# Kernel tuning notes

Hardware: AMD Instinct MI355X
Metric: run time of the kernel (lower is better)

Reference implementation:

```python
import jax, jax.numpy as jnp
import numpy as np

EPS = 1e-8
ITERATIONS = 3

def squash(s):
    # s: [b, j, m]
    s2 = jnp.sum(s * s, axis=-1, keepdims=True)
    return s2 / (1.0 + s2) * (s / jnp.sqrt(s2 + EPS))

def setup_inputs() -> dict:
    key = jax.random.key(0)
    k1, k2 = jax.random.split(key)
    B, NUMS_CAPS, OUT_CAPS, IN_D, OUT_D = 128, 1152, 10, 8, 16
    x = jax.random.normal(k1, (B, NUMS_CAPS, IN_D), dtype=jnp.float32)
    w = jax.random.normal(k2, (NUMS_CAPS, OUT_CAPS, IN_D, OUT_D), dtype=jnp.float32)
    return {"nums_caps": NUMS_CAPS, "out_caps": OUT_CAPS, "x": x, "w": w}

def reference(nums_caps, out_caps, x, w):
    # x: [b, i, n], w: [i, j, n, m] -> u_hat: [b, i, j, m]
    u_hat = jnp.einsum('ijnm,bin->bijm', w, x)
    b = jnp.zeros((x.shape[0], nums_caps, out_caps), dtype=x.dtype)
    v = None
    for _ in range(ITERATIONS):
        c = jax.nn.softmax(b, axis=1)  # softmax over input capsules (dim=1, as in source)
        s = jnp.einsum('bij,bijm->bjm', c, u_hat)
        v = squash(s)
        a = jnp.einsum('bjm,bijm->bij', v, u_hat)
        b = b + a
    return v
```

## Files before the change

kernel.cpp:

```cpp
#include <hip/hip_runtime.h>
#include <hip/hip_fp16.h>


#define NB 128
#define NI 1152
#define NJ 10
#define ID 8
#define OD 16

template<int ctrl, int rmask, int bmask>
__device__ __forceinline__ float dpp_add(float x) {
    int y = __builtin_amdgcn_update_dpp(0, __builtin_bit_cast(int, x),
                                        ctrl, rmask, bmask, false);
    return x + __builtin_bit_cast(float, y);
}
__device__ __forceinline__ float wave_sum63(float x) {
    x = dpp_add<0x111, 0xf, 0xf>(x);
    x = dpp_add<0x112, 0xf, 0xf>(x);
    x = dpp_add<0x114, 0xf, 0xe>(x);
    x = dpp_add<0x118, 0xf, 0xc>(x);
    x = dpp_add<0x142, 0xa, 0xf>(x);
    x = dpp_add<0x143, 0xc, 0xf>(x);
    return x;
}

__global__ __launch_bounds__(256) void uhat_kernel(
    const float* __restrict__ x, const float* __restrict__ w,
    __half* __restrict__ uhat)
{
    __shared__ float xl[16 * 640];
    const int t  = threadIdx.x;
    const int i0 = blockIdx.x * 64;
    const int b0 = blockIdx.y * 16;
    const int j  = blockIdx.z;

    #pragma unroll
    for (int c = 0; c < 8; ++c) {
        const int h  = t + 256 * c;
        const int bb = h >> 7;
        const int ii = (h >> 1) & 63;
        const int nh = h & 1;
        const float4 xv4 = *(const float4*)(
            x + ((size_t)(b0 + bb) * NI + (i0 + ii)) * ID + nh * 4);
        float* dst = &xl[bb * 640 + ii * 10 + nh * 4];
        dst[0] = xv4.x; dst[1] = xv4.y; dst[2] = xv4.z; dst[3] = xv4.w;
    }

    const int lane = t & 63;
    const int il   = (t >> 6) * 16 + (lane >> 2);
    const int i    = i0 + il;
    const int mq   = lane & 3;

    const float* wp = w + ((size_t)i * NJ + j) * (ID * OD) + mq * 4;
    float wr[8][4];
    #pragma unroll
    for (int n = 0; n < 8; ++n)
        *(float4*)wr[n] = *(const float4*)(wp + n * OD);

    __syncthreads();

    for (int bb = 0; bb < 16; ++bb) {
        const float* xr = &xl[bb * 640 + il * 10];
        float xv[ID];
        #pragma unroll
        for (int q = 0; q < 4; ++q) { xv[2*q] = xr[2*q]; xv[2*q+1] = xr[2*q+1]; }
        float a0 = 0.f, a1 = 0.f, a2 = 0.f, a3 = 0.f;
        #pragma unroll
        for (int n = 0; n < ID; ++n) {
            a0 = fmaf(xv[n], wr[n][0], a0);
            a1 = fmaf(xv[n], wr[n][1], a1);
            a2 = fmaf(xv[n], wr[n][2], a2);
            a3 = fmaf(xv[n], wr[n][3], a3);
        }
        __half2 h01 = __floats2half2_rn(a0, a1);
        __half2 h23 = __floats2half2_rn(a2, a3);
        uint2 st;
        st.x = *(unsigned int*)&h01;
        st.y = *(unsigned int*)&h23;
        __half* up = uhat + (((size_t)(b0 + bb) * NJ + j) * NI + i) * OD + mq * 4;
        *(uint2*)up = st;
    }
}

#define P2T 192
#define P2I 6

template<int NT, int IPTT>
__device__ __forceinline__ void route_core(float (&u)[IPTT][OD], int t, int b, int j,
                                           float* __restrict__ out)
{
    constexpr int NW = NT / 64;
    __shared__ float4 red4[NW][5];
    const int wavei = t >> 6;
    const int lane  = t & 63;

    float logit[IPTT];
    #pragma unroll
    for (int k = 0; k < IPTT; ++k) logit[k] = 0.0f;
    float v[OD];

    for (int iter = 0; iter < 3; ++iter) {
        float acc[OD + 1];
        #pragma unroll
        for (int q = 0; q <= OD; ++q) acc[q] = 0.0f;
        #pragma unroll
        for (int k = 0; k < IPTT; ++k) {
            const float c = __expf(logit[k]);
            acc[OD] += c;
            #pragma unroll
            for (int m = 0; m < OD; ++m) acc[m] = fmaf(c, u[k][m], acc[m]);
        }
        #pragma unroll
        for (int q = 0; q <= OD; ++q) acc[q] = wave_sum63(acc[q]);

        if (iter != 0) __syncthreads();
        if (lane == 63) {
            red4[wavei][0] = make_float4(acc[0],  acc[1],  acc[2],  acc[3]);
            red4[wavei][1] = make_float4(acc[4],  acc[5],  acc[6],  acc[7]);
            red4[wavei][2] = make_float4(acc[8],  acc[9],  acc[10], acc[11]);
            red4[wavei][3] = make_float4(acc[12], acc[13], acc[14], acc[15]);
            red4[wavei][4] = make_float4(acc[16], 0.f, 0.f, 0.f);
        }
        __syncthreads();

        float tot[OD + 1];
        #pragma unroll
        for (int g = 0; g < 5; ++g) {
            float4 sum = red4[0][g];
            #pragma unroll
            for (int wv = 1; wv < NW; ++wv) {
                float4 r = red4[wv][g];
                sum.x += r.x; sum.y += r.y; sum.z += r.z; sum.w += r.w;
            }
            if (g < 4) {
                tot[4*g+0] = sum.x; tot[4*g+1] = sum.y;
                tot[4*g+2] = sum.z; tot[4*g+3] = sum.w;
            } else {
                tot[OD] = sum.x;
            }
        }

        const float inv_den = 1.0f / tot[OD];
        float s2 = 0.0f;
        float sv[OD];
        #pragma unroll
        for (int m = 0; m < OD; ++m) {
            sv[m] = tot[m] * inv_den;
            s2 = fmaf(sv[m], sv[m], s2);
        }
        const float scale = (s2 / (1.0f + s2)) / sqrtf(s2 + 1e-8f);
        #pragma unroll
        for (int m = 0; m < OD; ++m) v[m] = scale * sv[m];

        if (iter < 2) {
            #pragma unroll
            for (int k = 0; k < IPTT; ++k) {
                float a = 0.0f;
                #pragma unroll
                for (int m = 0; m < OD; ++m) a = fmaf(v[m], u[k][m], a);
                logit[k] += a;
            }
        }
    }
    if (t < OD) out[((size_t)b * NJ + j) * OD + t] = v[t];
}

__global__ __launch_bounds__(P2T) void route_kernel(
    const __half* __restrict__ uhat, float* __restrict__ out)
{
    const int t = threadIdx.x;
    const int b = blockIdx.x & (NB - 1);
    const int j = blockIdx.x >> 7;

    const __half* upb = uhat + ((size_t)b * NJ + j) * NI * OD;
    float u[P2I][OD];
    #pragma unroll
    for (int k = 0; k < P2I; ++k) {
        const __half* p = upb + (size_t)(t + k * P2T) * OD;
        __half2 hp[8];
        *(float4*)&hp[0] = *(const float4*)(p);
        *(float4*)&hp[4] = *(const float4*)(p + 8);
        #pragma unroll
        for (int q = 0; q < 8; ++q) {
            float2 f = __half22float2(hp[q]);
            u[k][2*q] = f.x; u[k][2*q+1] = f.y;
        }
    }
    route_core<P2T, P2I>(u, t, b, j, out);
}

__global__ __launch_bounds__(P2T) void fused_kernel(
    const float* __restrict__ x, const float* __restrict__ w,
    float* __restrict__ out)
{
    const int t = threadIdx.x;
    const int b = blockIdx.x & (NB - 1);
    const int j = blockIdx.x >> 7;

    float u[P2I][OD];
    #pragma unroll
    for (int k = 0; k < P2I; ++k) {
        const int i = t + k * P2T;
        const float* xp = x + ((size_t)b * NI + i) * ID;
        float xv[ID];
        const float4 x0 = *(const float4*)(xp);
        const float4 x1 = *(const float4*)(xp + 4);
        xv[0]=x0.x; xv[1]=x0.y; xv[2]=x0.z; xv[3]=x0.w;
        xv[4]=x1.x; xv[5]=x1.y; xv[6]=x1.z; xv[7]=x1.w;
        const float* wp = w + ((size_t)i * NJ + j) * (ID * OD);
        #pragma unroll
        for (int m = 0; m < OD; ++m) u[k][m] = 0.0f;
        #pragma unroll
        for (int n = 0; n < ID; ++n) {
            float wrow[OD];
            *(float4*)(wrow + 0)  = *(const float4*)(wp + n * OD + 0);
            *(float4*)(wrow + 4)  = *(const float4*)(wp + n * OD + 4);
            *(float4*)(wrow + 8)  = *(const float4*)(wp + n * OD + 8);
            *(float4*)(wrow + 12) = *(const float4*)(wp + n * OD + 12);
            const float xn = xv[n];
            #pragma unroll
            for (int m = 0; m < OD; ++m) u[k][m] = fmaf(xn, wrow[m], u[k][m]);
        }
    }
    route_core<P2T, P2I>(u, t, b, j, out);
}

extern "C" void kernel_launch(void* const* d_in, const int* in_sizes, int n_in,
                              void* d_out, int out_size, void* d_ws, size_t ws_size,
                              hipStream_t stream) {
    const float* x = (const float*)d_in[2];
    const float* w = (const float*)d_in[3];
    float* out = (float*)d_out;

    const size_t UHAT_BYTES = (size_t)NB * NJ * NI * OD * sizeof(__half);

    if (ws_size >= UHAT_BYTES) {
        __half* uhat = (__half*)d_ws;
        hipLaunchKernelGGL(uhat_kernel, dim3(NI / 64, NB / 16, NJ), dim3(256),
                           0, stream, x, w, uhat);
        hipLaunchKernelGGL(route_kernel, dim3(NB * NJ), dim3(P2T),
                           0, stream, uhat, out);
    } else {
        hipLaunchKernelGGL(fused_kernel, dim3(NB * NJ), dim3(P2T),
                           0, stream, x, w, out);
    }
}
```

Baseline: 39.39 us.

## Route each (b,j) pair with a single wavefront, dropping block-level reduction

Replaces the 192-thread-per-pair routing kernel with one where each 64-lane wavefront handles a whole (b,j) pair and holds 18 capsules per lane as packed halves. Reductions use DPP plus readlane with no shared memory or __syncthreads. The first iteration skips the exp because all logits are zero. In exchange, register pressure rises (18x8 half2 registers plus logits) and each lane does more serial work, which may reduce occupancy.

```diff
diff --git a/kernel.cpp b/kernel.cpp
--- a/kernel.cpp
+++ b/kernel.cpp
@@ -22,6 +22,10 @@
     x = dpp_add<0x142, 0xa, 0xf>(x);
     x = dpp_add<0x143, 0xc, 0xf>(x);
     return x;
+}
+__device__ __forceinline__ float readlane63(float x) {
+    return __builtin_bit_cast(float,
+        __builtin_amdgcn_readlane(__builtin_bit_cast(int, x), 63));
 }
 
 __global__ __launch_bounds__(256) void uhat_kernel(
@@ -82,6 +86,85 @@
     }
 }
 
+#define WIPT 18
+
+__global__ __launch_bounds__(256) void route_wave_kernel(
+    const __half* __restrict__ uhat, float* __restrict__ out)
+{
+    const int t    = threadIdx.x;
+    const int lane = t & 63;
+    const int pair = blockIdx.x * 4 + (t >> 6);
+    const int b    = pair & (NB - 1);
+    const int j    = pair >> 7;
+
+    const __half* upb = uhat + (((size_t)b * NJ + j) * NI + lane) * OD;
+    __half2 uh[WIPT][8];
+    #pragma unroll
+    for (int k = 0; k < WIPT; ++k) {
+        const __half* p = upb + (size_t)k * 64 * OD;
+        *(float4*)&uh[k][0] = *(const float4*)(p);
+        *(float4*)&uh[k][4] = *(const float4*)(p + 8);
+    }
+
+    float logit[WIPT];
+    #pragma unroll
+    for (int k = 0; k < WIPT; ++k) logit[k] = 0.0f;
+
+    float vs[OD];
+
+    #pragma unroll 1
+    for (int iter = 0; iter < 3; ++iter) {
+        float acc[OD + 1];
+        #pragma unroll
+        for (int q = 0; q <= OD; ++q) acc[q] = 0.0f;
+        #pragma unroll
+        for (int k = 0; k < WIPT; ++k) {
+            const float c = (iter == 0) ? 1.0f : __expf(logit[k]);
+            acc[OD] += c;
+            #pragma unroll
+            for (int q = 0; q < 8; ++q) {
+                acc[2*q]   = fmaf(c, __low2float(uh[k][q]),  acc[2*q]);
+                acc[2*q+1] = fmaf(c, __high2float(uh[k][q]), acc[2*q+1]);
+            }
+        }
+        float tot[OD + 1];
+        #pragma unroll
+        for (int q = 0; q <= OD; ++q) tot[q] = readlane63(wave_sum63(acc[q]));
+
+        const float inv_den = 1.0f / tot[OD];
+        float s2 = 0.0f;
+        #pragma unroll
+        for (int m = 0; m < OD; ++m) {
+            vs[m] = tot[m] * inv_den;
+            s2 = fmaf(vs[m], vs[m], s2);
+        }
+        const float scale = (s2 / (1.0f + s2)) / sqrtf(s2 + 1e-8f);
+        #pragma unroll
+        for (int m = 0; m < OD; ++m) vs[m] *= scale;
+
+        if (iter < 2) {
+            #pragma unroll
+            for (int k = 0; k < WIPT; ++k) {
+                float a = 0.0f;
+                #pragma unroll
+                for (int q = 0; q < 8; ++q) {
+                    a = fmaf(vs[2*q],   __low2float(uh[k][q]),  a);
+                    a = fmaf(vs[2*q+1], __high2float(uh[k][q]), a);
+                }
+                logit[k] += a;
+            }
+        }
+    }
+
+    if (lane == 0) {
+        float* op = out + ((size_t)b * NJ + j) * OD;
+        *(float4*)(op + 0)  = make_float4(vs[0],  vs[1],  vs[2],  vs[3]);
+        *(float4*)(op + 4)  = make_float4(vs[4],  vs[5],  vs[6],  vs[7]);
+        *(float4*)(op + 8)  = make_float4(vs[8],  vs[9],  vs[10], vs[11]);
+        *(float4*)(op + 12) = make_float4(vs[12], vs[13], vs[14], vs[15]);
+    }
+}
+
 #define P2T 192
 #define P2I 6
 
@@ -163,30 +246,6 @@
         }
     }
     if (t < OD) out[((size_t)b * NJ + j) * OD + t] = v[t];
-}
-
-__global__ __launch_bounds__(P2T) void route_kernel(
-    const __half* __restrict__ uhat, float* __restrict__ out)
-{
-    const int t = threadIdx.x;
-    const int b = blockIdx.x & (NB - 1);
-    const int j = blockIdx.x >> 7;
-
-    const __half* upb = uhat + ((size_t)b * NJ + j) * NI * OD;
-    float u[P2I][OD];
-    #pragma unroll
-    for (int k = 0; k < P2I; ++k) {
-        const __half* p = upb + (size_t)(t + k * P2T) * OD;
-        __half2 hp[8];
-        *(float4*)&hp[0] = *(const float4*)(p);
-        *(float4*)&hp[4] = *(const float4*)(p + 8);
-        #pragma unroll
-        for (int q = 0; q < 8; ++q) {
-            float2 f = __half22float2(hp[q]);
-            u[k][2*q] = f.x; u[k][2*q+1] = f.y;
-        }
-    }
-    route_core<P2T, P2I>(u, t, b, j, out);
 }
 
 __global__ __launch_bounds__(P2T) void fused_kernel(
@@ -238,7 +297,7 @@
         __half* uhat = (__half*)d_ws;
         hipLaunchKernelGGL(uhat_kernel, dim3(NI / 64, NB / 16, NJ), dim3(256),
                            0, stream, x, w, uhat);
-        hipLaunchKernelGGL(route_kernel, dim3(NB * NJ), dim3(P2T),
+        hipLaunchKernelGGL(route_wave_kernel, dim3(NB * NJ / 4), dim3(256),
                            0, stream, uhat, out);
     } else {
         hipLaunchKernelGGL(fused_kernel, dim3(NB * NJ), dim3(P2T),
```

Result: slower. 41.96 us (+6.5%).
